# Optimization experiments

Hardware: AMD Instinct MI355X
Metric: run time of the kernel (lower is better)

## Reference

```python
import jax, jax.numpy as jnp
import numpy as np

N = 50000   # nodes
E = 800000  # edges (before self loops)
D = 128     # feature dim (n_feat == all n_units due to fusion-cat constraint)
BN_EPS = 1e-5


def _gcn_norm(edge_index, edge_weight, n):
    # PyG gcn_norm with add_self_loops=True (self-loop weight 1.0)
    loop = jnp.arange(n)
    row = jnp.concatenate([edge_index[0], loop])
    col = jnp.concatenate([edge_index[1], loop])
    w = jnp.concatenate([edge_weight, jnp.ones((n,), edge_weight.dtype)])
    deg = jax.ops.segment_sum(w, col, num_segments=n)  # [N]
    deg_safe = jnp.where(deg > 0, deg, 1.0)
    dis = jnp.where(deg > 0, jax.lax.rsqrt(deg_safe), 0.0)
    norm = dis[row] * w * dis[col]  # [E+N]
    return row, col, norm


def _gcn_conv(x, row, col, norm, W, b):
    # out_i = sum_{j->i} norm_ij * (x_j @ W) + b
    h = x @ W                                   # [N, Dout]
    msg = norm[:, None] * h[row]                # gather + scale, [E+N, Dout]
    out = jax.ops.segment_sum(msg, col, num_segments=x.shape[0])
    return out + b


def setup_inputs() -> dict:
    key = jax.random.key(0)
    ks = jax.random.split(key, 9)
    emb = jax.random.normal(ks[0], (N, D), jnp.float32)
    edge_index = jax.random.randint(ks[1], (2, E), 0, N)
    edge_weight = jax.random.uniform(ks[2], (E,), jnp.float32)
    W0 = jax.random.normal(ks[3], (D, D), jnp.float32) / np.sqrt(D).astype(np.float32)
    b0 = jnp.zeros((D,), jnp.float32)
    W1 = jax.random.normal(ks[4], (D, D), jnp.float32) / np.sqrt(D).astype(np.float32)
    b1 = jnp.zeros((D,), jnp.float32)
    bn_gamma = jax.random.uniform(ks[5], (D,), jnp.float32, 0.5, 1.5)
    bn_beta = jax.random.normal(ks[6], (D,), jnp.float32) * 0.1
    bn_mean = jax.random.normal(ks[7], (D,), jnp.float32) * 0.1
    bn_var = jax.random.uniform(ks[8], (D,), jnp.float32, 0.5, 1.5)
    return dict(emb=emb, edge_index=edge_index, edge_weight=edge_weight,
                W0=W0, b0=b0, W1=W1, b1=b1,
                bn_gamma=bn_gamma, bn_beta=bn_beta, bn_mean=bn_mean, bn_var=bn_var)


def reference(emb, edge_index, edge_weight, W0, b0, W1, b1,
              bn_gamma, bn_beta, bn_mean, bn_var):
    n = emb.shape[0]
    row, col, norm = _gcn_norm(edge_index, edge_weight, n)
    # loop runs once (batchnorm_stack has len 1 -> zip truncates):
    h1 = _gcn_conv(emb, row, col, norm, W0, b0)
    h1 = (h1 - bn_mean) * jax.lax.rsqrt(bn_var + BN_EPS) * bn_gamma + bn_beta
    h1 = jax.nn.elu(h1)  # dropout is identity in eval mode
    # final layer applied outside loop, no BN/ELU:
    h2 = _gcn_conv(h1, row, col, norm, W1, b1)
    # fusion: mean over [emb, h1, h2] along the stacked scale axis
    return (emb + h1 + h2) / 3.0
```

## Files before the change

kernel.cpp:

```cpp
#include <hip/hip_runtime.h>
#include <hip/hip_fp16.h>
#include <math.h>

#define BN_EPS 1e-5f
#define CAP 48
#define W_SCALE 68719476736.0f

typedef __attribute__((ext_vector_type(8))) short bf16x8;
typedef __attribute__((ext_vector_type(4))) float f32x4;

__device__ __forceinline__ unsigned short f2b(float f) {
    unsigned u = __float_as_uint(f);
    return (unsigned short)((u + 0x7fffu + ((u >> 16) & 1u)) >> 16);
}
__device__ __forceinline__ unsigned pack2(float lo, float hi) {
    return (unsigned)f2b(lo) | ((unsigned)f2b(hi) << 16);
}
__device__ __forceinline__ float slot_w(unsigned s) {
    return __half2float(__ushort_as_half((unsigned short)(s & 0xffffu)));
}
__device__ __forceinline__ float4 b2f4(ushort4 u) {
    return make_float4(__uint_as_float((unsigned)u.x << 16),
                       __uint_as_float((unsigned)u.y << 16),
                       __uint_as_float((unsigned)u.z << 16),
                       __uint_as_float((unsigned)u.w << 16));
}

__global__ __launch_bounds__(256) void k_pack(const float* __restrict__ W0,
                                              const float* __restrict__ W1,
                                              const float* __restrict__ emb,
                                              unsigned short* __restrict__ wp0,
                                              unsigned short* __restrict__ wp1,
                                              unsigned short* __restrict__ embB, int n) {
    int b = blockIdx.x;
    if (b < 16) {
        int tid = b * 256 + threadIdx.x;
        const float* W = (tid < 2048) ? W0 : W1;
        unsigned short* wp = (tid < 2048) ? wp0 : wp1;
        int f = tid & 2047;
        int q = f >> 9;
        int t = (f >> 6) & 7;
        int l = f & 63;
        int col = t * 16 + (l & 15);
        int k0 = q * 32 + (l >> 4) * 8;
        unsigned short o[8];
        #pragma unroll
        for (int j = 0; j < 8; ++j) o[j] = f2b(W[(k0 + j) * 128 + col]);
        *(uint4*)(wp + (size_t)f * 8) = *(uint4*)o;
    } else {
        int idx = (b - 16) * 256 + threadIdx.x;
        if (idx < n * 16) {
            const float4* src = (const float4*)emb + (size_t)idx * 2;
            float4 v0 = src[0], v1 = src[1];
            uint4 o;
            o.x = pack2(v0.x, v0.y); o.y = pack2(v0.z, v0.w);
            o.z = pack2(v1.x, v1.y); o.w = pack2(v1.z, v1.w);
            ((uint4*)embB)[idx] = o;
        }
    }
}

__global__ __launch_bounds__(256) void k_scatter(const int* __restrict__ erow,
                                                 const int* __restrict__ ecol,
                                                 const float* __restrict__ ew,
                                                 unsigned long long* __restrict__ packed,
                                                 unsigned* __restrict__ eEdge, int E) {
    int e0 = (blockIdx.x * 256 + threadIdx.x) * 4;
    if (e0 >= E) return;
    if (e0 + 3 < E) {
        int4 r4 = *(const int4*)(erow + e0);
        int4 c4 = *(const int4*)(ecol + e0);
        float4 w4 = *(const float4*)(ew + e0);
        unsigned long long i0 = (1ull << 44) | (unsigned long long)(w4.x * W_SCALE);
        unsigned long long i1 = (1ull << 44) | (unsigned long long)(w4.y * W_SCALE);
        unsigned long long i2 = (1ull << 44) | (unsigned long long)(w4.z * W_SCALE);
        unsigned long long i3 = (1ull << 44) | (unsigned long long)(w4.w * W_SCALE);
        unsigned h0 = __half_as_ushort(__float2half(w4.x));
        unsigned h1 = __half_as_ushort(__float2half(w4.y));
        unsigned h2 = __half_as_ushort(__float2half(w4.z));
        unsigned h3 = __half_as_ushort(__float2half(w4.w));
        unsigned p0 = (unsigned)(atomicAdd(&packed[(size_t)c4.x * 8], i0) >> 44);
        unsigned p1 = (unsigned)(atomicAdd(&packed[(size_t)c4.y * 8], i1) >> 44);
        unsigned p2 = (unsigned)(atomicAdd(&packed[(size_t)c4.z * 8], i2) >> 44);
        unsigned p3 = (unsigned)(atomicAdd(&packed[(size_t)c4.w * 8], i3) >> 44);
        if (p0 < CAP) __builtin_nontemporal_store(((unsigned)r4.x << 16) | h0,
                                                  &eEdge[(size_t)c4.x * CAP + p0]);
        if (p1 < CAP) __builtin_nontemporal_store(((unsigned)r4.y << 16) | h1,
                                                  &eEdge[(size_t)c4.y * CAP + p1]);
        if (p2 < CAP) __builtin_nontemporal_store(((unsigned)r4.z << 16) | h2,
                                                  &eEdge[(size_t)c4.z * CAP + p2]);
        if (p3 < CAP) __builtin_nontemporal_store(((unsigned)r4.w << 16) | h3,
                                                  &eEdge[(size_t)c4.w * CAP + p3]);
    } else {
        for (int e = e0; e < E; ++e) {
            int r = erow[e], c = ecol[e];
            float wv = ew[e];
            unsigned long long inc = (1ull << 44) | (unsigned long long)(wv * W_SCALE);
            unsigned hb = __half_as_ushort(__float2half(wv));
            unsigned p = (unsigned)(atomicAdd(&packed[(size_t)c * 8], inc) >> 44);
            if (p < CAP) __builtin_nontemporal_store(((unsigned)r << 16) | hb,
                                                     &eEdge[(size_t)c * CAP + p]);
        }
    }
}

__global__ __launch_bounds__(256) void k_dis(const unsigned long long* __restrict__ packed,
                                             float* __restrict__ dis,
                                             int* __restrict__ cnt, int n) {
    int i = blockIdx.x * 256 + threadIdx.x;
    if (i >= n) return;
    unsigned long long pk = packed[(size_t)i * 8];
    int c = (int)(pk >> 44);
    if (c > CAP) c = CAP;
    float deg = (float)((double)(pk & ((1ull << 44) - 1)) * (1.0 / 68719476736.0));
    dis[i] = rsqrtf(deg + 1.0f);
    cnt[i] = c;
}

__device__ __forceinline__ void agg_node(const unsigned* __restrict__ ep,
                                         const unsigned short* __restrict__ h,
                                         const float* __restrict__ dis,
                                         float disc, int c, int lane,
                                         float acc[8]) {
    int g = lane >> 4;
    int fo = (lane & 15) * 8;
    for (int j = 0; j < c; j += 16) {
        unsigned s[4];
        int r[4];
        float d[4], nm[4];
        uint4 u[4];
        #pragma unroll
        for (int k = 0; k < 4; ++k) s[k] = ep[j + 4 * k + g];
        #pragma unroll
        for (int k = 0; k < 4; ++k) r[k] = (j + 4 * k + g < c) ? (int)(s[k] >> 16) : 0;
        #pragma unroll
        for (int k = 0; k < 4; ++k) d[k] = dis[r[k]];
        #pragma unroll
        for (int k = 0; k < 4; ++k) u[k] = *(const uint4*)(h + ((size_t)r[k] << 7) + fo);
        #pragma unroll
        for (int k = 0; k < 4; ++k)
            nm[k] = (j + 4 * k + g < c) ? d[k] * slot_w(s[k]) * disc : 0.f;
        #pragma unroll
        for (int k = 0; k < 4; ++k) {
            acc[0] += nm[k] * __uint_as_float(u[k].x << 16);
            acc[1] += nm[k] * __uint_as_float(u[k].x & 0xffff0000u);
            acc[2] += nm[k] * __uint_as_float(u[k].y << 16);
            acc[3] += nm[k] * __uint_as_float(u[k].y & 0xffff0000u);
            acc[4] += nm[k] * __uint_as_float(u[k].z << 16);
            acc[5] += nm[k] * __uint_as_float(u[k].z & 0xffff0000u);
            acc[6] += nm[k] * __uint_as_float(u[k].w << 16);
            acc[7] += nm[k] * __uint_as_float(u[k].w & 0xffff0000u);
        }
    }
    #pragma unroll
    for (int f = 0; f < 8; ++f) {
        acc[f] += __shfl_xor(acc[f], 16);
        acc[f] += __shfl_xor(acc[f], 32);
    }
}

__global__ __launch_bounds__(1024) void k_conv1(
        const int* __restrict__ cnt, const unsigned* __restrict__ eEdge,
        const unsigned short* __restrict__ embB, const float* __restrict__ dis,
        const unsigned short* __restrict__ wp,
        const float* __restrict__ b0, const float* __restrict__ gamma,
        const float* __restrict__ beta, const float* __restrict__ mean,
        const float* __restrict__ var,
        unsigned short* __restrict__ h1b, int n) {
    __shared__ unsigned short sWp[16384];
    __shared__ unsigned short sA[16 * 136];
    int t = threadIdx.x;
    { uint4* d = (uint4*)sWp; const uint4* s = (const uint4*)wp;
      d[t] = s[t]; d[t + 1024] = s[t + 1024]; }
    int w = t >> 6;
    int lane = t & 63;
    int wid = blockIdx.x * 16 + w;
    bool valid = wid < n;
    int c = valid ? __builtin_amdgcn_readfirstlane(cnt[wid]) : 0;
    float disc = valid ? dis[wid] : 0.f;
    float acc[8] = {};
    agg_node(eEdge + (size_t)wid * CAP, embB, dis, disc, c, lane, acc);
    if (lane < 16) {
        int fo = lane * 8;
        float s2 = disc * disc;
        uint4 hu = make_uint4(0, 0, 0, 0);
        if (valid) hu = *(const uint4*)(embB + ((size_t)wid << 7) + fo);
        acc[0] += s2 * __uint_as_float(hu.x << 16);
        acc[1] += s2 * __uint_as_float(hu.x & 0xffff0000u);
        acc[2] += s2 * __uint_as_float(hu.y << 16);
        acc[3] += s2 * __uint_as_float(hu.y & 0xffff0000u);
        acc[4] += s2 * __uint_as_float(hu.z << 16);
        acc[5] += s2 * __uint_as_float(hu.z & 0xffff0000u);
        acc[6] += s2 * __uint_as_float(hu.w << 16);
        acc[7] += s2 * __uint_as_float(hu.w & 0xffff0000u);
        uint4 o;
        o.x = pack2(acc[0], acc[1]); o.y = pack2(acc[2], acc[3]);
        o.z = pack2(acc[4], acc[5]); o.w = pack2(acc[6], acc[7]);
        *(uint4*)(sA + w * 136 + fo) = o;
    }
    __syncthreads();
    int m = lane & 15, quad = lane >> 4;
    f32x4 c2 = {0.f, 0.f, 0.f, 0.f};
    if (w < 8) {
        #pragma unroll
        for (int q = 0; q < 4; ++q) {
            bf16x8 a = *(const bf16x8*)(sA + m * 136 + q * 32 + quad * 8);
            bf16x8 b = *(const bf16x8*)(sWp + (size_t)((q * 8 + w) * 64 + lane) * 8);
            c2 = __builtin_amdgcn_mfma_f32_16x16x32_bf16(a, b, c2, 0, 0, 0);
        }
    }
    __syncthreads();
    if (w < 8) {
        int col = w * 16 + m;
        float bias = b0[col];
        float mn = mean[col], bt = beta[col];
        float iv = rsqrtf(var[col] + BN_EPS) * gamma[col];
        #pragma unroll
        for (int r = 0; r < 4; ++r) {
            float x = c2[r] + bias;
            x = (x - mn) * iv + bt;
            x = x > 0.f ? x : expm1f(x);
            sA[(quad * 4 + r) * 136 + col] = f2b(x);
        }
    }
    __syncthreads();
    if (t < 256) {
        int r = t >> 4, c8 = (t & 15) * 8;
        int node = blockIdx.x * 16 + r;
        if (node < n)
            *(uint4*)(h1b + ((size_t)node << 7) + c8) = *(const uint4*)(sA + r * 136 + c8);
    }
}

__global__ __launch_bounds__(1024) void k_conv2(
        const int* __restrict__ cnt, const unsigned* __restrict__ eEdge,
        const unsigned short* __restrict__ h1b, const float* __restrict__ dis,
        const unsigned short* __restrict__ wp,
        const float* __restrict__ b1, const float* __restrict__ emb,
        float* __restrict__ out, int n) {
    __shared__ unsigned short sWp[16384];
    __shared__ unsigned short sA[16 * 136];
    __shared__ float sC[16 * 132];
    int t = threadIdx.x;
    { uint4* d = (uint4*)sWp; const uint4* s = (const uint4*)wp;
      d[t] = s[t]; d[t + 1024] = s[t + 1024]; }
    int w = t >> 6;
    int lane = t & 63;
    int wid = blockIdx.x * 16 + w;
    bool valid = wid < n;
    int c = valid ? __builtin_amdgcn_readfirstlane(cnt[wid]) : 0;
    float disc = valid ? dis[wid] : 0.f;
    float acc[8] = {};
    agg_node(eEdge + (size_t)wid * CAP, h1b, dis, disc, c, lane, acc);
    if (lane < 16) {
        int fo = lane * 8;
        float s2 = disc * disc;
        uint4 hu = make_uint4(0, 0, 0, 0);
        if (valid) hu = *(const uint4*)(h1b + ((size_t)wid << 7) + fo);
        acc[0] += s2 * __uint_as_float(hu.x << 16);
        acc[1] += s2 * __uint_as_float(hu.x & 0xffff0000u);
        acc[2] += s2 * __uint_as_float(hu.y << 16);
        acc[3] += s2 * __uint_as_float(hu.y & 0xffff0000u);
        acc[4] += s2 * __uint_as_float(hu.z << 16);
        acc[5] += s2 * __uint_as_float(hu.z & 0xffff0000u);
        acc[6] += s2 * __uint_as_float(hu.w << 16);
        acc[7] += s2 * __uint_as_float(hu.w & 0xffff0000u);
        uint4 o;
        o.x = pack2(acc[0], acc[1]); o.y = pack2(acc[2], acc[3]);
        o.z = pack2(acc[4], acc[5]); o.w = pack2(acc[6], acc[7]);
        *(uint4*)(sA + w * 136 + fo) = o;
    }
    __syncthreads();
    int m = lane & 15, quad = lane >> 4;
    f32x4 c2 = {0.f, 0.f, 0.f, 0.f};
    if (w < 8) {
        #pragma unroll
        for (int q = 0; q < 4; ++q) {
            bf16x8 a = *(const bf16x8*)(sA + m * 136 + q * 32 + quad * 8);
            bf16x8 b = *(const bf16x8*)(sWp + (size_t)((q * 8 + w) * 64 + lane) * 8);
            c2 = __builtin_amdgcn_mfma_f32_16x16x32_bf16(a, b, c2, 0, 0, 0);
        }
        int col = w * 16 + m;
        float bias = b1[col];
        #pragma unroll
        for (int r = 0; r < 4; ++r)
            sC[(quad * 4 + r) * 132 + col] = c2[r] + bias;
    }
    __syncthreads();
    if (t < 512) {
        int r = t >> 5, c4 = (t & 31) * 4;
        int node = blockIdx.x * 16 + r;
        if (node < n) {
            float4 cc = *(const float4*)(sC + r * 132 + c4);
            float4 ev = *(const float4*)(emb + ((size_t)node << 7) + c4);
            float4 hv = b2f4(*(const ushort4*)(h1b + ((size_t)node << 7) + c4));
            const float third = 1.0f / 3.0f;
            float4 o;
            o.x = (ev.x + hv.x + cc.x) * third;
            o.y = (ev.y + hv.y + cc.y) * third;
            o.z = (ev.z + hv.z + cc.z) * third;
            o.w = (ev.w + hv.w + cc.w) * third;
            *(float4*)(out + ((size_t)node << 7) + c4) = o;
        }
    }
}

extern "C" void kernel_launch(void* const* d_in, const int* in_sizes, int n_in,
                              void* d_out, int out_size, void* d_ws, size_t ws_size,
                              hipStream_t stream) {
    const float* emb   = (const float*)d_in[0];
    const int*   eidx  = (const int*)d_in[1];
    const float* ew    = (const float*)d_in[2];
    const float* W0    = (const float*)d_in[3];
    const float* b0    = (const float*)d_in[4];
    const float* W1    = (const float*)d_in[5];
    const float* b1    = (const float*)d_in[6];
    const float* gamma = (const float*)d_in[7];
    const float* beta  = (const float*)d_in[8];
    const float* mean  = (const float*)d_in[9];
    const float* var   = (const float*)d_in[10];

    const int n = in_sizes[0] / 128;
    const int E = in_sizes[2];
    const int* rowp = eidx;
    const int* colp = eidx + E;

    char* ws = (char*)d_ws;
    unsigned short* embB = (unsigned short*)ws;
    unsigned short* h1b  = (unsigned short*)(ws + (size_t)n * 256);
    char* p = ws + (size_t)n * 512;
    unsigned long long* packed = (unsigned long long*)p;
    float* dis  = (float*)(p + (size_t)n * 64);
    int*   cnt  = (int*)  (p + (size_t)n * 68);
    unsigned short* wp0 = (unsigned short*)(p + (size_t)n * 72);
    unsigned short* wp1 = (unsigned short*)(p + (size_t)n * 72 + 32768);
    unsigned* eEdge = (unsigned*)(p + (size_t)n * 72 + 65536);
    float* outf = (float*)d_out;

    hipMemsetAsync(packed, 0, (size_t)n * 64, stream);

    const int nb = (n + 255) / 256;
    const int sb = (E + 1023) / 1024;
    const int pb = 16 + (n * 16 + 255) / 256;
    const int cb = (n + 15) / 16;

    k_pack<<<pb, 256, 0, stream>>>(W0, W1, emb, wp0, wp1, embB, n);
    k_scatter<<<sb, 256, 0, stream>>>(rowp, colp, ew, packed, eEdge, E);
    k_dis<<<nb, 256, 0, stream>>>(packed, dis, cnt, n);
    k_conv1<<<cb, 1024, 0, stream>>>(cnt, eEdge, embB, dis, wp0,
                                     b0, gamma, beta, mean, var, h1b, n);
    k_conv2<<<cb, 1024, 0, stream>>>(cnt, eEdge, h1b, dis, wp1,
                                     b1, emb, outf, n);
}
```

Before: 244.3 us.

## Merge scatter into pack kernel and compute degree from stored edge weights

Fuses the edge-scatter kernel with the weight/embedding packing kernel into a single launch. The 64-bit packed count+weight-sum atomic becomes a 32-bit count-only atomic. The weighted degree is then recomputed in k_dis by a per-node wave reduction over the fp16 weights stored in the edge slots. This removes one launch and shrinks atomic width, but the degree now uses fp16-rounded weights and only the first CAP edges, which changes numerics for nodes that overflow.

```diff
diff --git a/kernel.cpp b/kernel.cpp
--- a/kernel.cpp
+++ b/kernel.cpp
@@ -4,7 +4,6 @@
 
 #define BN_EPS 1e-5f
 #define CAP 48
-#define W_SCALE 68719476736.0f
 
 typedef __attribute__((ext_vector_type(8))) short bf16x8;
 typedef __attribute__((ext_vector_type(4))) float f32x4;
@@ -26,15 +25,53 @@
                        __uint_as_float((unsigned)u.w << 16));
 }
 
-__global__ __launch_bounds__(256) void k_pack(const float* __restrict__ W0,
+__global__ __launch_bounds__(256) void k_prep(const int* __restrict__ erow,
+                                              const int* __restrict__ ecol,
+                                              const float* __restrict__ ew,
+                                              unsigned* __restrict__ cntPad,
+                                              unsigned* __restrict__ eEdge, int E,
+                                              const float* __restrict__ W0,
                                               const float* __restrict__ W1,
                                               const float* __restrict__ emb,
                                               unsigned short* __restrict__ wp0,
                                               unsigned short* __restrict__ wp1,
-                                              unsigned short* __restrict__ embB, int n) {
+                                              unsigned short* __restrict__ embB,
+                                              int n, int sb) {
     int b = blockIdx.x;
-    if (b < 16) {
-        int tid = b * 256 + threadIdx.x;
+    if (b < sb) {
+        int e0 = (b * 256 + threadIdx.x) * 4;
+        if (e0 >= E) return;
+        if (e0 + 3 < E) {
+            int4 r4 = *(const int4*)(erow + e0);
+            int4 c4 = *(const int4*)(ecol + e0);
+            float4 w4 = *(const float4*)(ew + e0);
+            unsigned h0 = __half_as_ushort(__float2half(w4.x));
+            unsigned h1 = __half_as_ushort(__float2half(w4.y));
+            unsigned h2 = __half_as_ushort(__float2half(w4.z));
+            unsigned h3 = __half_as_ushort(__float2half(w4.w));
+            unsigned p0 = atomicAdd(&cntPad[(size_t)c4.x * 16], 1u);
+            unsigned p1 = atomicAdd(&cntPad[(size_t)c4.y * 16], 1u);
+            unsigned p2 = atomicAdd(&cntPad[(size_t)c4.z * 16], 1u);
+            unsigned p3 = atomicAdd(&cntPad[(size_t)c4.w * 16], 1u);
+            if (p0 < CAP) __builtin_nontemporal_store(((unsigned)r4.x << 16) | h0,
+                                                      &eEdge[(size_t)c4.x * CAP + p0]);
+            if (p1 < CAP) __builtin_nontemporal_store(((unsigned)r4.y << 16) | h1,
+                                                      &eEdge[(size_t)c4.y * CAP + p1]);
+            if (p2 < CAP) __builtin_nontemporal_store(((unsigned)r4.z << 16) | h2,
+                                                      &eEdge[(size_t)c4.z * CAP + p2]);
+            if (p3 < CAP) __builtin_nontemporal_store(((unsigned)r4.w << 16) | h3,
+                                                      &eEdge[(size_t)c4.w * CAP + p3]);
+        } else {
+            for (int e = e0; e < E; ++e) {
+                int r = erow[e], c = ecol[e];
+                unsigned hb = __half_as_ushort(__float2half(ew[e]));
+                unsigned p = atomicAdd(&cntPad[(size_t)c * 16], 1u);
+                if (p < CAP) __builtin_nontemporal_store(((unsigned)r << 16) | hb,
+                                                         &eEdge[(size_t)c * CAP + p]);
+            }
+        }
+    } else if (b < sb + 16) {
+        int tid = (b - sb) * 256 + threadIdx.x;
         const float* W = (tid < 2048) ? W0 : W1;
         unsigned short* wp = (tid < 2048) ? wp0 : wp1;
         int f = tid & 2047;
@@ -48,7 +85,7 @@
         for (int j = 0; j < 8; ++j) o[j] = f2b(W[(k0 + j) * 128 + col]);
         *(uint4*)(wp + (size_t)f * 8) = *(uint4*)o;
     } else {
-        int idx = (b - 16) * 256 + threadIdx.x;
+        int idx = (b - sb - 16) * 256 + threadIdx.x;
         if (idx < n * 16) {
             const float4* src = (const float4*)emb + (size_t)idx * 2;
             float4 v0 = src[0], v1 = src[1];
@@ -60,61 +97,23 @@
     }
 }
 
-__global__ __launch_bounds__(256) void k_scatter(const int* __restrict__ erow,
-                                                 const int* __restrict__ ecol,
-                                                 const float* __restrict__ ew,
-                                                 unsigned long long* __restrict__ packed,
-                                                 unsigned* __restrict__ eEdge, int E) {
-    int e0 = (blockIdx.x * 256 + threadIdx.x) * 4;
-    if (e0 >= E) return;
-    if (e0 + 3 < E) {
-        int4 r4 = *(const int4*)(erow + e0);
-        int4 c4 = *(const int4*)(ecol + e0);
-        float4 w4 = *(const float4*)(ew + e0);
-        unsigned long long i0 = (1ull << 44) | (unsigned long long)(w4.x * W_SCALE);
-        unsigned long long i1 = (1ull << 44) | (unsigned long long)(w4.y * W_SCALE);
-        unsigned long long i2 = (1ull << 44) | (unsigned long long)(w4.z * W_SCALE);
-        unsigned long long i3 = (1ull << 44) | (unsigned long long)(w4.w * W_SCALE);
-        unsigned h0 = __half_as_ushort(__float2half(w4.x));
-        unsigned h1 = __half_as_ushort(__float2half(w4.y));
-        unsigned h2 = __half_as_ushort(__float2half(w4.z));
-        unsigned h3 = __half_as_ushort(__float2half(w4.w));
-        unsigned p0 = (unsigned)(atomicAdd(&packed[(size_t)c4.x * 8], i0) >> 44);
-        unsigned p1 = (unsigned)(atomicAdd(&packed[(size_t)c4.y * 8], i1) >> 44);
-        unsigned p2 = (unsigned)(atomicAdd(&packed[(size_t)c4.z * 8], i2) >> 44);
-        unsigned p3 = (unsigned)(atomicAdd(&packed[(size_t)c4.w * 8], i3) >> 44);
-        if (p0 < CAP) __builtin_nontemporal_store(((unsigned)r4.x << 16) | h0,
-                                                  &eEdge[(size_t)c4.x * CAP + p0]);
-        if (p1 < CAP) __builtin_nontemporal_store(((unsigned)r4.y << 16) | h1,
-                                                  &eEdge[(size_t)c4.y * CAP + p1]);
-        if (p2 < CAP) __builtin_nontemporal_store(((unsigned)r4.z << 16) | h2,
-                                                  &eEdge[(size_t)c4.z * CAP + p2]);
-        if (p3 < CAP) __builtin_nontemporal_store(((unsigned)r4.w << 16) | h3,
-                                                  &eEdge[(size_t)c4.w * CAP + p3]);
-    } else {
-        for (int e = e0; e < E; ++e) {
-            int r = erow[e], c = ecol[e];
-            float wv = ew[e];
-            unsigned long long inc = (1ull << 44) | (unsigned long long)(wv * W_SCALE);
-            unsigned hb = __half_as_ushort(__float2half(wv));
-            unsigned p = (unsigned)(atomicAdd(&packed[(size_t)c * 8], inc) >> 44);
-            if (p < CAP) __builtin_nontemporal_store(((unsigned)r << 16) | hb,
-                                                     &eEdge[(size_t)c * CAP + p]);
-        }
-    }
-}
-
-__global__ __launch_bounds__(256) void k_dis(const unsigned long long* __restrict__ packed,
+__global__ __launch_bounds__(256) void k_dis(const unsigned* __restrict__ cntPad,
                                              float* __restrict__ dis,
-                                             int* __restrict__ cnt, int n) {
-    int i = blockIdx.x * 256 + threadIdx.x;
-    if (i >= n) return;
-    unsigned long long pk = packed[(size_t)i * 8];
-    int c = (int)(pk >> 44);
+                                             int* __restrict__ cnt,
+                                             const unsigned* __restrict__ eEdge, int n) {
+    int wid = (blockIdx.x * 256 + threadIdx.x) >> 6;
+    if (wid >= n) return;
+    int lane = threadIdx.x & 63;
+    int c = __builtin_amdgcn_readfirstlane((int)cntPad[(size_t)wid * 16]);
     if (c > CAP) c = CAP;
-    float deg = (float)((double)(pk & ((1ull << 44) - 1)) * (1.0 / 68719476736.0));
-    dis[i] = rsqrtf(deg + 1.0f);
-    cnt[i] = c;
+    float wsum = 0.f;
+    if (lane < c) wsum = slot_w(eEdge[(size_t)wid * CAP + lane]);
+    #pragma unroll
+    for (int off = 32; off; off >>= 1) wsum += __shfl_xor(wsum, off);
+    if (lane == 0) {
+        dis[wid] = rsqrtf(wsum + 1.0f);
+        cnt[wid] = c;
+    }
 }
 
 __device__ __forceinline__ void agg_node(const unsigned* __restrict__ ep,
@@ -329,7 +328,7 @@
     unsigned short* embB = (unsigned short*)ws;
     unsigned short* h1b  = (unsigned short*)(ws + (size_t)n * 256);
     char* p = ws + (size_t)n * 512;
-    unsigned long long* packed = (unsigned long long*)p;
+    unsigned* cntPad = (unsigned*)p;
     float* dis  = (float*)(p + (size_t)n * 64);
     int*   cnt  = (int*)  (p + (size_t)n * 68);
     unsigned short* wp0 = (unsigned short*)(p + (size_t)n * 72);
@@ -337,16 +336,16 @@
     unsigned* eEdge = (unsigned*)(p + (size_t)n * 72 + 65536);
     float* outf = (float*)d_out;
 
-    hipMemsetAsync(packed, 0, (size_t)n * 64, stream);
-
-    const int nb = (n + 255) / 256;
+    hipMemsetAsync(cntPad, 0, (size_t)n * 64, stream);
+
     const int sb = (E + 1023) / 1024;
-    const int pb = 16 + (n * 16 + 255) / 256;
+    const int pb = sb + 16 + (n * 16 + 255) / 256;
+    const int wb = (int)(((size_t)n * 64 + 255) / 256);
     const int cb = (n + 15) / 16;
 
-    k_pack<<<pb, 256, 0, stream>>>(W0, W1, emb, wp0, wp1, embB, n);
-    k_scatter<<<sb, 256, 0, stream>>>(rowp, colp, ew, packed, eEdge, E);
-    k_dis<<<nb, 256, 0, stream>>>(packed, dis, cnt, n);
+    k_prep<<<pb, 256, 0, stream>>>(rowp, colp, ew, cntPad, eEdge, E,
+                                   W0, W1, emb, wp0, wp1, embB, n, sb);
+    k_dis<<<wb, 256, 0, stream>>>(cntPad, dis, cnt, eEdge, n);
     k_conv1<<<cb, 1024, 0, stream>>>(cnt, eEdge, embB, dis, wp0,
                                      b0, gamma, beta, mean, var, h1b, n);
     k_conv2<<<cb, 1024, 0, stream>>>(cnt, eEdge, h1b, dis, wp1,
```

Result: slower. 264.2 us (+8.2%).
